# Kernel optimization log

Hardware: AMD Instinct MI355X
Metric: run time of the kernel (lower is better)

The kernel has to match this reference:

```python
import jax, jax.numpy as jnp
import numpy as np

DIM = 512
HEADS = 8
HEAD_DIM = DIM // HEADS
SCALE = DIM ** (-0.5)  # source uses full dim, not head_dim
LAMBDA_COND = 1.0


def setup_inputs() -> dict:
    key = jax.random.key(0)
    ks = jax.random.split(key, 16)
    b, n, m_a, m_s = 4, 2048, 2048, 256
    s = 0.02
    inp = {
        "x": jax.random.normal(ks[0], (b, n, DIM), jnp.float32),
        "audio_context": jax.random.normal(ks[1], (b, m_a, DIM), jnp.float32),
        "singer_context": jax.random.normal(ks[2], (b, m_s, DIM), jnp.float32),
        "Wq": jax.random.normal(ks[3], (DIM, DIM), jnp.float32) * s,
        "bq": jnp.zeros((DIM,), jnp.float32),
        "Wka": jax.random.normal(ks[4], (DIM, DIM), jnp.float32) * s,
        "bka": jnp.zeros((DIM,), jnp.float32),
        "Wva": jax.random.normal(ks[5], (DIM, DIM), jnp.float32) * s,
        "bva": jnp.zeros((DIM,), jnp.float32),
        "Wks": jax.random.normal(ks[6], (DIM, DIM), jnp.float32) * s,
        "bks": jnp.zeros((DIM,), jnp.float32),
        "Wvs": jax.random.normal(ks[7], (DIM, DIM), jnp.float32) * s,
        "bvs": jnp.zeros((DIM,), jnp.float32),
        "Wp": jax.random.normal(ks[8], (DIM, DIM), jnp.float32) * s,
        "bp": jnp.zeros((DIM,), jnp.float32),
    }
    return inp


def _heads(t):
    b, n, c = t.shape
    return t.reshape(b, n, HEADS, HEAD_DIM).transpose(0, 2, 1, 3)  # (b,h,n,d)


def _attend(q, ctx, Wk, bk, Wv, bv):
    k = _heads(ctx @ Wk.T + bk)
    v = _heads(ctx @ Wv.T + bv)
    attn = jax.nn.softmax(jnp.einsum("bhnd,bhmd->bhnm", q, k) * SCALE, axis=-1)
    o = jnp.einsum("bhnm,bhmd->bhnd", attn, v)
    b, h, n, d = o.shape
    return o.transpose(0, 2, 1, 3).reshape(b, n, h * d)


def reference(x, audio_context, singer_context, Wq, bq, Wka, bka, Wva, bva,
              Wks, bks, Wvs, bvs, Wp, bp):
    q = _heads(x @ Wq.T + bq)
    x_audio = _attend(q, audio_context, Wka, bka, Wva, bva)
    x_singer = _attend(q, singer_context, Wks, bks, Wvs, bvs)
    out = x_audio + LAMBDA_COND * x_singer
    return out @ Wp.T + bp
```

## Files before the change

### kernel.cpp

```cpp
#include <hip/hip_runtime.h>

#define DIM 512
#define NQ 2048
#define MA 2048
#define MS 256
#define QSCALE 0.06375864651f

typedef __attribute__((ext_vector_type(8))) short bf16x8;
typedef __attribute__((ext_vector_type(4))) float f32x4;
typedef __attribute__((ext_vector_type(16))) float f32x16;

__device__ __forceinline__ ushort f2b(float f) {
    uint u = __float_as_uint(f);
    u = (u + 0x7fffu + ((u >> 16) & 1u)) >> 16;
    return (ushort)u;
}

__device__ __forceinline__ void gload16(const ushort* g, ushort* l) {
    __builtin_amdgcn_global_load_lds(
        (const __attribute__((address_space(1))) void*)g,
        (__attribute__((address_space(3))) void*)l, 16, 0, 0);
}

__global__ __launch_bounds__(256) void cast_all(const float* __restrict__ w0,
                                                const float* __restrict__ w1,
                                                const float* __restrict__ w2,
                                                const float* __restrict__ w3,
                                                const float* __restrict__ w4,
                                                const float* __restrict__ w5,
                                                const float* __restrict__ x,
                                                const float* __restrict__ ac,
                                                const float* __restrict__ scx,
                                                ushort* __restrict__ dst) {
    int i = blockIdx.x * 256 + threadIdx.x;
    const float* s;
    int o;
    if (i < 393216) {
        int w = i >> 16;
        s = w < 3 ? (w == 0 ? w0 : (w == 1 ? w1 : w2))
                  : (w == 3 ? w3 : (w == 4 ? w4 : w5));
        o = i & 65535;
    } else if (i < 1441792) { s = x;   o = i - 393216; }
    else if (i < 2490368)   { s = ac;  o = i - 1441792; }
    else                    { s = scx; o = i - 2490368; }
    float4 v = ((const float4*)s)[o];
    ushort4 u;
    u.x = f2b(v.x); u.y = f2b(v.y); u.z = f2b(v.z); u.w = f2b(v.w);
    ((ushort4*)dst)[i] = u;
}

struct GD {
    const ushort* A; const ushort* B; const float* bias; void* out;
    long sB, sO;
    int N, bx, by, blk0, biasrow, scaleq, outf32, pad;
};

__global__ __launch_bounds__(256) void gemm_fused(GD d0, GD d1, GD d2, GD d3, GD d4) {
    __shared__ ushort At[128 * 32];
    __shared__ ushort Bt[128 * 32];
    GD d = d0;
    int bid = blockIdx.x;
    if (bid >= d1.blk0) d = d1;
    if (bid >= d2.blk0) d = d2;
    if (bid >= d3.blk0) d = d3;
    if (bid >= d4.blk0) d = d4;
    int local = bid - d.blk0;
    int x = local % d.bx;
    int rem = local / d.bx;
    int y = rem % d.by;
    int z = rem / d.by;

    int t = threadIdx.x;
    int wv = t >> 6, ln = t & 63, l = ln & 15, g = ln >> 4;
    int wrow = wv & 1, wcol = wv >> 1;
    int row0 = x * 128, col0 = y * 128;
    int srow = t >> 2;
    int slot = (t & 3) * 8;
    int sko = ((t ^ srow) & 3) * 8;
    int kc8 = ((g ^ (l & 3)) & 3) * 8;
    const ushort* Ab = d.A;
    const ushort* Bb = d.B + (size_t)z * d.sB;
    int N = d.N;

    f32x4 acc[4][4];
#pragma unroll
    for (int i = 0; i < 4; i++)
#pragma unroll
        for (int j = 0; j < 4; j++) acc[i][j] = (f32x4){0, 0, 0, 0};

    for (int k0 = 0; k0 < 512; k0 += 32) {
        __syncthreads();
#pragma unroll
        for (int c = 0; c < 2; c++) {
            gload16(Ab + (size_t)(row0 + srow + 64 * c) * 512 + k0 + sko,
                    At + (srow + 64 * c) * 32 + slot);
            gload16(Bb + (size_t)(col0 + srow + 64 * c) * 512 + k0 + sko,
                    Bt + (srow + 64 * c) * 32 + slot);
        }
        __syncthreads();
        bf16x8 ar[4], br[4];
#pragma unroll
        for (int i = 0; i < 4; i++)
            ar[i] = *(const bf16x8*)(At + (wrow * 64 + i * 16 + l) * 32 + kc8);
#pragma unroll
        for (int j = 0; j < 4; j++)
            br[j] = *(const bf16x8*)(Bt + (wcol * 64 + j * 16 + l) * 32 + kc8);
#pragma unroll
        for (int i = 0; i < 4; i++)
#pragma unroll
            for (int j = 0; j < 4; j++)
                acc[i][j] = __builtin_amdgcn_mfma_f32_16x16x32_bf16(ar[i], br[j], acc[i][j], 0, 0, 0);
    }
#pragma unroll
    for (int i = 0; i < 4; i++) {
#pragma unroll
        for (int j = 0; j < 4; j++) {
            int row = row0 + wrow * 64 + i * 16 + g * 4;
            int col = col0 + wcol * 64 + j * 16 + l;
#pragma unroll
            for (int r = 0; r < 4; r++) {
                float bv = d.biasrow ? d.bias[row + r] : d.bias[col];
                float o = acc[i][j][r] + bv;
                if (d.scaleq) o *= QSCALE;
                if (d.outf32)
                    ((float*)d.out + (size_t)z * d.sO)[(size_t)(row + r) * N + col] = o;
                else
                    ((ushort*)d.out + (size_t)z * d.sO)[(size_t)(row + r) * N + col] = f2b(o);
            }
        }
    }
}

__device__ __forceinline__ void attn_ctx32(const ushort* __restrict__ kg,
                                           const ushort* __restrict__ vg,
                                           int M, const bf16x8 (&aq)[4],
                                           ushort* __restrict__ Kl,
                                           ushort* __restrict__ Vl,
                                           ushort* __restrict__ Pw,
                                           f32x16 (&o)[2], float& li,
                                           int l5, int hi, int sr, int sc) {
    bf16x8 k0 = *(const bf16x8*)kg;
    bf16x8 k1 = *(const bf16x8*)(kg + (size_t)32 * DIM);
    bf16x8 v0 = *(const bf16x8*)vg;
    bf16x8 v1 = *(const bf16x8*)(vg + (size_t)32 * M);
    for (int mt = 0; mt < M; mt += 64) {
        __syncthreads();
        *(bf16x8*)(Kl + sr * 72 + sc) = k0;
        *(bf16x8*)(Kl + (sr + 32) * 72 + sc) = k1;
        *(bf16x8*)(Vl + sr * 72 + sc) = v0;
        *(bf16x8*)(Vl + (sr + 32) * 72 + sc) = v1;
        __syncthreads();
        if (mt + 64 < M) {
            k0 = *(const bf16x8*)(kg + (size_t)(mt + 64) * DIM);
            k1 = *(const bf16x8*)(kg + (size_t)(mt + 96) * DIM);
            v0 = *(const bf16x8*)(vg + (mt + 64));
            v1 = *(const bf16x8*)(vg + (size_t)32 * M + (mt + 64));
        }
#pragma unroll
        for (int c = 0; c < 2; c++) {
            f32x16 s;
#pragma unroll
            for (int i = 0; i < 16; i++) s[i] = 0.f;
#pragma unroll
            for (int kd = 0; kd < 4; kd++) {
                bf16x8 kf = *(const bf16x8*)(Kl + (32 * c + l5) * 72 + kd * 16 + hi * 8);
                s = __builtin_amdgcn_mfma_f32_32x32x16_bf16(kf, aq[kd], s, 0, 0, 0);
            }
#pragma unroll
            for (int m = 0; m < 4; m++) {
                float p0 = exp2f(s[4 * m + 0]);
                float p1 = exp2f(s[4 * m + 1]);
                float p2 = exp2f(s[4 * m + 2]);
                float p3 = exp2f(s[4 * m + 3]);
                li += (p0 + p1) + (p2 + p3);
                uint2 pw;
                pw.x = ((__float_as_uint(p0) + 0x8000u) >> 16) |
                       ((__float_as_uint(p1) + 0x8000u) & 0xffff0000u);
                pw.y = ((__float_as_uint(p2) + 0x8000u) >> 16) |
                       ((__float_as_uint(p3) + 0x8000u) & 0xffff0000u);
                *(uint2*)(Pw + l5 * 72 + 32 * c + 8 * m + 4 * hi) = pw;
            }
        }
        bf16x8 pf[4];
#pragma unroll
        for (int kc = 0; kc < 4; kc++)
            pf[kc] = *(const bf16x8*)(Pw + l5 * 72 + kc * 16 + hi * 8);
#pragma unroll
        for (int dn = 0; dn < 2; dn++)
#pragma unroll
            for (int kc = 0; kc < 4; kc++) {
                bf16x8 vf = *(const bf16x8*)(Vl + (32 * dn + l5) * 72 + kc * 16 + hi * 8);
                o[dn] = __builtin_amdgcn_mfma_f32_32x32x16_bf16(pf[kc], vf, o[dn], 0, 0, 0);
            }
    }
}

__global__ __launch_bounds__(256) void attn_kernel(const ushort* __restrict__ q,
                                                   const ushort* __restrict__ Ka,
                                                   const ushort* __restrict__ VTa,
                                                   const ushort* __restrict__ Ks,
                                                   const ushort* __restrict__ VTs,
                                                   ushort* __restrict__ y) {
    __shared__ ushort Kl[64 * 72];
    __shared__ ushort Vl[64 * 72];
    __shared__ ushort Pl[4 * 32 * 72];
    int t = threadIdx.x;
    int wv = t >> 6, ln = t & 63, l5 = ln & 31, hi = ln >> 5;
    int h = blockIdx.y, bi = blockIdx.z;
    int q0 = blockIdx.x * 128 + wv * 32;
    bf16x8 aq[4];
    const ushort* qp = q + (size_t)(bi * NQ + q0 + l5) * DIM + h * 64 + hi * 8;
#pragma unroll
    for (int kd = 0; kd < 4; kd++) aq[kd] = *(const bf16x8*)(qp + kd * 16);
    int sr = t >> 3, sc = (t & 7) * 8;
    ushort* Pw = Pl + wv * 32 * 72;

    f32x16 o[2];
#pragma unroll
    for (int dn = 0; dn < 2; dn++)
#pragma unroll
        for (int i = 0; i < 16; i++) o[dn][i] = 0.f;
    float li = 0.f;

    attn_ctx32(Ks + (size_t)bi * MS * DIM + (size_t)sr * DIM + h * 64 + sc,
               VTs + (size_t)bi * DIM * MS + (size_t)(h * 64 + sr) * MS + sc,
               MS, aq, Kl, Vl, Pw, o, li, l5, hi, sr, sc);
    li += __shfl_xor(li, 32);
    float inv[16];
#pragma unroll
    for (int rg = 0; rg < 16; rg++)
        inv[rg] = 1.f / __shfl(li, (rg & 3) + 8 * (rg >> 2) + 4 * hi);
    float yv[2][16];
#pragma unroll
    for (int dn = 0; dn < 2; dn++)
#pragma unroll
        for (int rg = 0; rg < 16; rg++) yv[dn][rg] = o[dn][rg] * inv[rg];

#pragma unroll
    for (int dn = 0; dn < 2; dn++)
#pragma unroll
        for (int i = 0; i < 16; i++) o[dn][i] = 0.f;
    li = 0.f;
    attn_ctx32(Ka + (size_t)bi * MA * DIM + (size_t)sr * DIM + h * 64 + sc,
               VTa + (size_t)bi * DIM * MA + (size_t)(h * 64 + sr) * MA + sc,
               MA, aq, Kl, Vl, Pw, o, li, l5, hi, sr, sc);
    li += __shfl_xor(li, 32);
#pragma unroll
    for (int rg = 0; rg < 16; rg++)
        inv[rg] = 1.f / __shfl(li, (rg & 3) + 8 * (rg >> 2) + 4 * hi);

#pragma unroll
    for (int dn = 0; dn < 2; dn++)
#pragma unroll
        for (int rg = 0; rg < 16; rg++) {
            int qr = (rg & 3) + 8 * (rg >> 2) + 4 * hi;
            float ov = yv[dn][rg] + o[dn][rg] * inv[rg];
            y[(size_t)(bi * NQ + q0 + qr) * DIM + h * 64 + 32 * dn + l5] = f2b(ov);
        }
}

extern "C" void kernel_launch(void* const* d_in, const int* in_sizes, int n_in,
                              void* d_out, int out_size, void* d_ws, size_t ws_size,
                              hipStream_t stream) {
    const float* x   = (const float*)d_in[0];
    const float* ac  = (const float*)d_in[1];
    const float* scx = (const float*)d_in[2];
    const float* Wq  = (const float*)d_in[3];
    const float* bq  = (const float*)d_in[4];
    const float* Wka = (const float*)d_in[5];
    const float* bka = (const float*)d_in[6];
    const float* Wva = (const float*)d_in[7];
    const float* bva = (const float*)d_in[8];
    const float* Wks = (const float*)d_in[9];
    const float* bks = (const float*)d_in[10];
    const float* Wvs = (const float*)d_in[11];
    const float* bvs = (const float*)d_in[12];
    const float* Wp  = (const float*)d_in[13];
    const float* bp  = (const float*)d_in[14];

    ushort* wb   = (ushort*)d_ws;
    ushort* wqb  = wb;
    ushort* wkab = wb + 262144;
    ushort* wvab = wb + 2 * 262144;
    ushort* wksb = wb + 3 * 262144;
    ushort* wvsb = wb + 4 * 262144;
    ushort* wpb  = wb + 5 * 262144;
    ushort* xb   = wb + 6 * 262144;
    ushort* acb  = xb + 4194304;
    ushort* scxb = acb + 4194304;
    ushort* qb   = scxb + 524288;
    ushort* kab  = qb + 4194304;
    ushort* vta  = kab + 4194304;
    ushort* ksb  = vta + 4194304;
    ushort* vts  = ksb + 524288;
    ushort* yb   = xb;

    cast_all<<<10240, 256, 0, stream>>>(Wq, Wka, Wva, Wks, Wvs, Wp, x, ac, scx, wb);

    GD gq   = {xb,   wqb,  bq,  qb,  0, 0,               512,  64, 4,  0,   0, 1, 0, 0};
    GD gka  = {acb,  wkab, bka, kab, 0, 0,               512,  64, 4,  256, 0, 0, 0, 0};
    GD gvta = {wvab, acb,  bva, vta, 2048L * 512, 512L * 2048, 2048, 4, 16, 512, 1, 0, 0, 0};
    GD gks  = {scxb, wksb, bks, ksb, 0, 0,               512,  8,  4,  768, 0, 0, 0, 0};
    GD gvts = {wvsb, scxb, bvs, vts, 256L * 512, 512L * 256,   256,  4,  2,  800, 1, 0, 0, 0};
    gemm_fused<<<832, 256, 0, stream>>>(gq, gka, gvta, gks, gvts);

    attn_kernel<<<dim3(16, 8, 4), 256, 0, stream>>>(qb, kab, vta, ksb, vts, yb);

    GD gpr = {yb, wpb, bp, d_out, 0, 0, 512, 64, 4, 0, 0, 0, 1, 0};
    GD gnv = {nullptr, nullptr, nullptr, nullptr, 0, 0, 0, 1, 1, 1 << 30, 0, 0, 0, 0};
    gemm_fused<<<256, 256, 0, stream>>>(gpr, gnv, gnv, gnv, gnv);
}
```

Before: 252.8 us.

## Load K/V fragments directly from global, widen GEMM K-tile, use packed bf16 convert

The attention kernel no longer stages K and V tiles through shared memory with block-wide barriers. Each wave now loads its MFMA fragments straight from global memory, relying on cache for reuse across the four waves. The projection GEMM doubles its K-step to 64 with an XOR-swizzled LDS layout, halving the number of barrier pairs. P is packed to bf16 with the hardware pack-convert instruction when the compiler provides it. The costs are redundant global/L2 traffic per wave in attention, no prefetch overlap for K/V, and round-to-nearest-even P conversion in place of the old biased rounding.

```diff
diff --git a/kernel.cpp b/kernel.cpp
--- a/kernel.cpp
+++ b/kernel.cpp
@@ -14,6 +14,19 @@
     uint u = __float_as_uint(f);
     u = (u + 0x7fffu + ((u >> 16) & 1u)) >> 16;
     return (ushort)u;
+}
+
+__device__ __forceinline__ uint pk2bf(float a, float b) {
+#if __has_builtin(__builtin_amdgcn_cvt_pk_bf16_f32)
+    typedef __attribute__((ext_vector_type(2))) __bf16 bf2;
+    bf2 r = __builtin_amdgcn_cvt_pk_bf16_f32(a, b);
+    uint u;
+    __builtin_memcpy(&u, &r, 4);
+    return u;
+#else
+    return ((__float_as_uint(a) + 0x8000u) >> 16) |
+           ((__float_as_uint(b) + 0x8000u) & 0xffff0000u);
+#endif
 }
 
 __device__ __forceinline__ void gload16(const ushort* g, ushort* l) {
@@ -56,8 +69,8 @@
 };
 
 __global__ __launch_bounds__(256) void gemm_fused(GD d0, GD d1, GD d2, GD d3, GD d4) {
-    __shared__ ushort At[128 * 32];
-    __shared__ ushort Bt[128 * 32];
+    __shared__ ushort At[128 * 64];
+    __shared__ ushort Bt[128 * 64];
     GD d = d0;
     int bid = blockIdx.x;
     if (bid >= d1.blk0) d = d1;
@@ -74,10 +87,8 @@
     int wv = t >> 6, ln = t & 63, l = ln & 15, g = ln >> 4;
     int wrow = wv & 1, wcol = wv >> 1;
     int row0 = x * 128, col0 = y * 128;
-    int srow = t >> 2;
-    int slot = (t & 3) * 8;
-    int sko = ((t ^ srow) & 3) * 8;
-    int kc8 = ((g ^ (l & 3)) & 3) * 8;
+    int srw = t >> 3;
+    int chs = ((t & 7) ^ ((t >> 3) & 7)) * 8;
     const ushort* Ab = d.A;
     const ushort* Bb = d.B + (size_t)z * d.sB;
     int N = d.N;
@@ -88,28 +99,31 @@
 #pragma unroll
         for (int j = 0; j < 4; j++) acc[i][j] = (f32x4){0, 0, 0, 0};
 
-    for (int k0 = 0; k0 < 512; k0 += 32) {
+    for (int k0 = 0; k0 < 512; k0 += 64) {
         __syncthreads();
 #pragma unroll
-        for (int c = 0; c < 2; c++) {
-            gload16(Ab + (size_t)(row0 + srow + 64 * c) * 512 + k0 + sko,
-                    At + (srow + 64 * c) * 32 + slot);
-            gload16(Bb + (size_t)(col0 + srow + 64 * c) * 512 + k0 + sko,
-                    Bt + (srow + 64 * c) * 32 + slot);
+        for (int j = 0; j < 4; j++) {
+            int r = j * 32 + srw;
+            gload16(Ab + (size_t)(row0 + r) * 512 + k0 + chs, At + j * 2048 + t * 8);
+            gload16(Bb + (size_t)(col0 + r) * 512 + k0 + chs, Bt + j * 2048 + t * 8);
         }
         __syncthreads();
-        bf16x8 ar[4], br[4];
-#pragma unroll
-        for (int i = 0; i < 4; i++)
-            ar[i] = *(const bf16x8*)(At + (wrow * 64 + i * 16 + l) * 32 + kc8);
-#pragma unroll
-        for (int j = 0; j < 4; j++)
-            br[j] = *(const bf16x8*)(Bt + (wcol * 64 + j * 16 + l) * 32 + kc8);
-#pragma unroll
-        for (int i = 0; i < 4; i++)
+#pragma unroll
+        for (int kb = 0; kb < 2; kb++) {
+            int rc = ((4 * kb + g) ^ (l & 7)) * 8;
+            bf16x8 ar[4], br[4];
+#pragma unroll
+            for (int i = 0; i < 4; i++)
+                ar[i] = *(const bf16x8*)(At + (wrow * 64 + i * 16 + l) * 64 + rc);
 #pragma unroll
             for (int j = 0; j < 4; j++)
-                acc[i][j] = __builtin_amdgcn_mfma_f32_16x16x32_bf16(ar[i], br[j], acc[i][j], 0, 0, 0);
+                br[j] = *(const bf16x8*)(Bt + (wcol * 64 + j * 16 + l) * 64 + rc);
+#pragma unroll
+            for (int i = 0; i < 4; i++)
+#pragma unroll
+                for (int j = 0; j < 4; j++)
+                    acc[i][j] = __builtin_amdgcn_mfma_f32_16x16x32_bf16(ar[i], br[j], acc[i][j], 0, 0, 0);
+        }
     }
 #pragma unroll
     for (int i = 0; i < 4; i++) {
@@ -131,41 +145,32 @@
     }
 }
 
-__device__ __forceinline__ void attn_ctx32(const ushort* __restrict__ kg,
-                                           const ushort* __restrict__ vg,
-                                           int M, const bf16x8 (&aq)[4],
-                                           ushort* __restrict__ Kl,
-                                           ushort* __restrict__ Vl,
+__device__ __forceinline__ void attn_ctx32(const ushort* __restrict__ kp,
+                                           const ushort* __restrict__ vp,
+                                           int M,
+                                           const bf16x8 (&aq)[4],
                                            ushort* __restrict__ Pw,
                                            f32x16 (&o)[2], float& li,
-                                           int l5, int hi, int sr, int sc) {
-    bf16x8 k0 = *(const bf16x8*)kg;
-    bf16x8 k1 = *(const bf16x8*)(kg + (size_t)32 * DIM);
-    bf16x8 v0 = *(const bf16x8*)vg;
-    bf16x8 v1 = *(const bf16x8*)(vg + (size_t)32 * M);
+                                           int l5, int hi) {
     for (int mt = 0; mt < M; mt += 64) {
-        __syncthreads();
-        *(bf16x8*)(Kl + sr * 72 + sc) = k0;
-        *(bf16x8*)(Kl + (sr + 32) * 72 + sc) = k1;
-        *(bf16x8*)(Vl + sr * 72 + sc) = v0;
-        *(bf16x8*)(Vl + (sr + 32) * 72 + sc) = v1;
-        __syncthreads();
-        if (mt + 64 < M) {
-            k0 = *(const bf16x8*)(kg + (size_t)(mt + 64) * DIM);
-            k1 = *(const bf16x8*)(kg + (size_t)(mt + 96) * DIM);
-            v0 = *(const bf16x8*)(vg + (mt + 64));
-            v1 = *(const bf16x8*)(vg + (size_t)32 * M + (mt + 64));
-        }
+        bf16x8 vf[2][4];
+#pragma unroll
+        for (int dn = 0; dn < 2; dn++)
+#pragma unroll
+            for (int kc = 0; kc < 4; kc++)
+                vf[dn][kc] = *(const bf16x8*)(vp + (size_t)(32 * dn) * M + mt + kc * 16);
 #pragma unroll
         for (int c = 0; c < 2; c++) {
+            bf16x8 kf[4];
+#pragma unroll
+            for (int kd = 0; kd < 4; kd++)
+                kf[kd] = *(const bf16x8*)(kp + (size_t)(mt + 32 * c) * DIM + kd * 16);
             f32x16 s;
 #pragma unroll
             for (int i = 0; i < 16; i++) s[i] = 0.f;
 #pragma unroll
-            for (int kd = 0; kd < 4; kd++) {
-                bf16x8 kf = *(const bf16x8*)(Kl + (32 * c + l5) * 72 + kd * 16 + hi * 8);
-                s = __builtin_amdgcn_mfma_f32_32x32x16_bf16(kf, aq[kd], s, 0, 0, 0);
-            }
+            for (int kd = 0; kd < 4; kd++)
+                s = __builtin_amdgcn_mfma_f32_32x32x16_bf16(kf[kd], aq[kd], s, 0, 0, 0);
 #pragma unroll
             for (int m = 0; m < 4; m++) {
                 float p0 = exp2f(s[4 * m + 0]);
@@ -174,10 +179,8 @@
                 float p3 = exp2f(s[4 * m + 3]);
                 li += (p0 + p1) + (p2 + p3);
                 uint2 pw;
-                pw.x = ((__float_as_uint(p0) + 0x8000u) >> 16) |
-                       ((__float_as_uint(p1) + 0x8000u) & 0xffff0000u);
-                pw.y = ((__float_as_uint(p2) + 0x8000u) >> 16) |
-                       ((__float_as_uint(p3) + 0x8000u) & 0xffff0000u);
+                pw.x = pk2bf(p0, p1);
+                pw.y = pk2bf(p2, p3);
                 *(uint2*)(Pw + l5 * 72 + 32 * c + 8 * m + 4 * hi) = pw;
             }
         }
@@ -188,10 +191,8 @@
 #pragma unroll
         for (int dn = 0; dn < 2; dn++)
 #pragma unroll
-            for (int kc = 0; kc < 4; kc++) {
-                bf16x8 vf = *(const bf16x8*)(Vl + (32 * dn + l5) * 72 + kc * 16 + hi * 8);
-                o[dn] = __builtin_amdgcn_mfma_f32_32x32x16_bf16(pf[kc], vf, o[dn], 0, 0, 0);
-            }
+            for (int kc = 0; kc < 4; kc++)
+                o[dn] = __builtin_amdgcn_mfma_f32_32x32x16_bf16(pf[kc], vf[dn][kc], o[dn], 0, 0, 0);
     }
 }
 
@@ -201,8 +202,6 @@
                                                    const ushort* __restrict__ Ks,
                                                    const ushort* __restrict__ VTs,
                                                    ushort* __restrict__ y) {
-    __shared__ ushort Kl[64 * 72];
-    __shared__ ushort Vl[64 * 72];
     __shared__ ushort Pl[4 * 32 * 72];
     int t = threadIdx.x;
     int wv = t >> 6, ln = t & 63, l5 = ln & 31, hi = ln >> 5;
@@ -212,7 +211,6 @@
     const ushort* qp = q + (size_t)(bi * NQ + q0 + l5) * DIM + h * 64 + hi * 8;
 #pragma unroll
     for (int kd = 0; kd < 4; kd++) aq[kd] = *(const bf16x8*)(qp + kd * 16);
-    int sr = t >> 3, sc = (t & 7) * 8;
     ushort* Pw = Pl + wv * 32 * 72;
 
     f32x16 o[2];
@@ -222,9 +220,9 @@
         for (int i = 0; i < 16; i++) o[dn][i] = 0.f;
     float li = 0.f;
 
-    attn_ctx32(Ks + (size_t)bi * MS * DIM + (size_t)sr * DIM + h * 64 + sc,
-               VTs + (size_t)bi * DIM * MS + (size_t)(h * 64 + sr) * MS + sc,
-               MS, aq, Kl, Vl, Pw, o, li, l5, hi, sr, sc);
+    const ushort* kps = Ks + (size_t)(bi * MS + l5) * DIM + h * 64 + hi * 8;
+    const ushort* vps = VTs + (size_t)bi * DIM * MS + (size_t)(h * 64 + l5) * MS + hi * 8;
+    attn_ctx32(kps, vps, MS, aq, Pw, o, li, l5, hi);
     li += __shfl_xor(li, 32);
     float inv[16];
 #pragma unroll
@@ -241,9 +239,9 @@
 #pragma unroll
         for (int i = 0; i < 16; i++) o[dn][i] = 0.f;
     li = 0.f;
-    attn_ctx32(Ka + (size_t)bi * MA * DIM + (size_t)sr * DIM + h * 64 + sc,
-               VTa + (size_t)bi * DIM * MA + (size_t)(h * 64 + sr) * MA + sc,
-               MA, aq, Kl, Vl, Pw, o, li, l5, hi, sr, sc);
+    const ushort* kpa = Ka + (size_t)(bi * MA + l5) * DIM + h * 64 + hi * 8;
+    const ushort* vpa = VTa + (size_t)bi * DIM * MA + (size_t)(h * 64 + l5) * MA + hi * 8;
+    attn_ctx32(kpa, vpa, MA, aq, Pw, o, li, l5, hi);
     li += __shfl_xor(li, 32);
 #pragma unroll
     for (int rg = 0; rg < 16; rg++)
```

Result: slower. 307.4 us (+21.6%).
